# Kernel optimization log

Measured on AMD Instinct MI355X. Metric: run time of the kernel, lower is better.

The kernel has to match this reference:

```python
import jax, jax.numpy as jnp
import numpy as np

D_MODEL = 1024
N_LAYERS = 2
D_STATE = 64
D_CONV = 4
EXPAND = 2
D_INNER = EXPAND * D_MODEL            # 2048
HEADDIM = D_STATE                     # 64 (headdim=d_state per module code)
NHEADS = D_INNER // HEADDIM           # 32
CONV_DIM = D_INNER + 2 * D_STATE      # 2176 (ngroups=1)
D_IN_PROJ = 2 * D_INNER + 2 * D_STATE + NHEADS  # 4256
EPS = 1e-5


def setup_inputs() -> dict:
    key = jax.random.key(0)
    ks = jax.random.split(key, 8)
    B, L = 2, 4096
    return {
        "x": jax.random.normal(ks[0], (B, L, D_MODEL), jnp.float32),
        "ln_w": jnp.ones((N_LAYERS, D_MODEL), jnp.float32),
        "ln_b": jnp.zeros((N_LAYERS, D_MODEL), jnp.float32),
        "in_proj_w": jax.random.normal(ks[1], (N_LAYERS, D_IN_PROJ, D_MODEL), jnp.float32) * (D_MODEL ** -0.5),
        "conv_w": jax.random.normal(ks[2], (N_LAYERS, CONV_DIM, D_CONV), jnp.float32) * (D_CONV ** -0.5),
        "conv_b": jnp.zeros((N_LAYERS, CONV_DIM), jnp.float32),
        "dt_bias": jax.random.normal(ks[3], (N_LAYERS, NHEADS), jnp.float32) * 0.5,
        "A_log": jnp.log(jax.random.uniform(ks[4], (N_LAYERS, NHEADS), jnp.float32, 1.0, 16.0)),
        "D": jnp.ones((N_LAYERS, NHEADS), jnp.float32),
        "rms_w": jnp.ones((N_LAYERS, D_INNER), jnp.float32),
        "out_proj_w": jax.random.normal(ks[5], (N_LAYERS, D_MODEL, D_INNER), jnp.float32) * (D_INNER ** -0.5),
    }


def _layernorm(x, w, b):
    m = x.mean(-1, keepdims=True)
    v = ((x - m) ** 2).mean(-1, keepdims=True)
    return (x - m) * jax.lax.rsqrt(v + EPS) * w + b


def _mamba2(u, in_w, conv_w, conv_b, dt_bias, A_log, Dp, rms_w, out_w):
    b, l, _ = u.shape
    zxbcdt = u @ in_w.T                                   # (b,l,D_IN_PROJ)
    z, xBC, dt = jnp.split(zxbcdt, [D_INNER, D_INNER + CONV_DIM], axis=-1)
    dt = jax.nn.softplus(dt + dt_bias)                    # (b,l,H)
    # causal depthwise conv over sequence
    xBC = jnp.transpose(xBC, (0, 2, 1))                   # (b,C,l)
    xBC = jax.lax.conv_general_dilated(
        xBC, conv_w[:, None, :], (1,), [(D_CONV - 1, 0)],
        dimension_numbers=("NCH", "OIH", "NCH"), feature_group_count=CONV_DIM)
    xBC = jnp.transpose(xBC, (0, 2, 1)) + conv_b
    xBC = jax.nn.silu(xBC)
    xh, Bm, Cm = jnp.split(xBC, [D_INNER, D_INNER + D_STATE], axis=-1)
    xh = xh.reshape(b, l, NHEADS, HEADDIM)                # (b,l,H,P)
    A = -jnp.exp(A_log)                                   # (H,)
    dA = jnp.exp(dt * A)                                  # (b,l,H)

    def step(state, inputs):
        dA_t, dt_t, x_t, B_t, C_t = inputs                # (b,H),(b,H),(b,H,P),(b,N),(b,N)
        state = dA_t[:, :, None, None] * state + (dt_t[:, :, None] * x_t)[..., None] * B_t[:, None, None, :]
        y_t = jnp.einsum("bhpn,bn->bhp", state, C_t)
        return state, y_t

    xs = (jnp.moveaxis(dA, 1, 0), jnp.moveaxis(dt, 1, 0), jnp.moveaxis(xh, 1, 0),
          jnp.moveaxis(Bm, 1, 0), jnp.moveaxis(Cm, 1, 0))
    init = jnp.zeros((b, NHEADS, HEADDIM, D_STATE), u.dtype)
    _, ys = jax.lax.scan(step, init, xs)                  # ys: (l,b,H,P)
    y = jnp.moveaxis(ys, 0, 1) + Dp[None, None, :, None] * xh
    y = y.reshape(b, l, D_INNER)
    # gated RMSNorm (norm_before_gate=False): gate then rmsnorm
    y = y * jax.nn.silu(z)
    y = y * jax.lax.rsqrt(jnp.mean(y * y, -1, keepdims=True) + EPS) * rms_w
    return y @ out_w.T


def reference(x, ln_w, ln_b, in_proj_w, conv_w, conv_b, dt_bias, A_log, D, rms_w, out_proj_w):
    h = x
    for i in range(N_LAYERS):
        res = h
        h = _layernorm(h, ln_w[i], ln_b[i])
        h = _mamba2(h, in_proj_w[i], conv_w[i], conv_b[i], dt_bias[i], A_log[i], D[i], rms_w[i], out_proj_w[i])
        h = h + res
    return h
```

## Files before the change

kernel.cpp:

```cpp
#include <hip/hip_runtime.h>
#include <stdint.h>

#define D_MODEL   1024
#define D_STATE   64
#define D_INNER   2048
#define NHEADS    32
#define CONV_DIM  2176
#define D_IN_PROJ 4256
#define NPAD1     4352
#define LSEQ      4096
#define BL        8192
#define NCHUNK    32
#define TCH       128
#define EPS       1e-5f

typedef __attribute__((ext_vector_type(8))) _Float16 f16x8;
typedef __attribute__((ext_vector_type(4))) _Float16 f16x4;
typedef __attribute__((ext_vector_type(4))) float f32x4;

__device__ __forceinline__ void load_lds16(const void* g, void* l) {
  __builtin_amdgcn_global_load_lds((const __attribute__((address_space(1))) void*)g,
                                   (__attribute__((address_space(3))) void*)l, 16, 0, 0);
}

__global__ __launch_bounds__(256) void cvt_w1_kernel(const float* __restrict__ w,
                                                     _Float16* __restrict__ o) {
  size_t idx = (size_t)blockIdx.x * 256 + threadIdx.x;
  int k = idx & 1023;
  size_t nr = idx >> 10;
  int layer = (int)(nr / NPAD1);
  int n = (int)(nr % NPAD1);
  float v = (n < D_IN_PROJ) ? w[((size_t)layer * D_IN_PROJ + n) * 1024 + k] : 0.f;
  o[idx] = (_Float16)v;
}
__global__ __launch_bounds__(256) void cvt_w2_kernel(const float* __restrict__ w,
                                                     _Float16* __restrict__ o) {
  size_t idx = (size_t)blockIdx.x * 256 + threadIdx.x;
  o[idx] = (_Float16)w[idx];
}

__global__ __launch_bounds__(256) void ln_kernel(const float* __restrict__ x,
                                                 const float* __restrict__ w,
                                                 const float* __restrict__ b,
                                                 _Float16* __restrict__ o) {
  int row = blockIdx.x, tid = threadIdx.x;
  const float* xr = x + (size_t)row * D_MODEL;
  float4 v = *(const float4*)(xr + tid * 4);
  float s = v.x + v.y + v.z + v.w;
  float q = v.x * v.x + v.y * v.y + v.z * v.z + v.w * v.w;
  for (int off = 1; off < 64; off <<= 1) { s += __shfl_xor(s, off); q += __shfl_xor(q, off); }
  __shared__ float rs[4], rq[4];
  int wave = tid >> 6, lane = tid & 63;
  if (lane == 0) { rs[wave] = s; rq[wave] = q; }
  __syncthreads();
  s = rs[0] + rs[1] + rs[2] + rs[3];
  q = rq[0] + rq[1] + rq[2] + rq[3];
  float mean = s * (1.f / D_MODEL);
  float var = q * (1.f / D_MODEL) - mean * mean;
  float rstd = rsqrtf(var + EPS);
  int c = tid * 4;
  f16x4 ov;
  ov[0] = (_Float16)((v.x - mean) * rstd * w[c + 0] + b[c + 0]);
  ov[1] = (_Float16)((v.y - mean) * rstd * w[c + 1] + b[c + 1]);
  ov[2] = (_Float16)((v.z - mean) * rstd * w[c + 2] + b[c + 2]);
  ov[3] = (_Float16)((v.w - mean) * rstd * w[c + 3] + b[c + 3]);
  *(f16x4*)(o + (size_t)row * D_MODEL + c) = ov;
}

template <int MODE>
__global__ __launch_bounds__(512, 4) void gemm_f16_kernel(
    const _Float16* __restrict__ A, int lda,
    const _Float16* __restrict__ Bw, int K, int NBN,
    _Float16* __restrict__ Zb, _Float16* __restrict__ XPRE, float* __restrict__ AUX,
    float* __restrict__ Cf, const float* __restrict__ resid) {
  __shared__ _Float16 lA[2][256 * 32];
  __shared__ _Float16 lB[2][128 * 32];
  int tid = threadIdx.x;
  int wv = tid >> 6, lane = tid & 63;
  int nwg = gridDim.x;
  int cpx = nwg >> 3;
  int wg = ((int)blockIdx.x & 7) * cpx + ((int)blockIdx.x >> 3);
  int band = wg / (4 * NBN), rem = wg % (4 * NBN);
  int bm = band * 4 + (rem & 3);
  int bn = rem >> 2;

  const int wm = (wv >> 1) * 64, wn = (wv & 1) * 64;
  const int fr = lane & 15;
  const int s4 = lane >> 4;
  size_t aoff = (size_t)(bm * 256) * lda;
  size_t boff = (size_t)(bn * 128) * K;

  f32x4 acc[4][4];
  f32x4 zero = {0.f, 0.f, 0.f, 0.f};
#pragma unroll
  for (int i = 0; i < 4; ++i)
#pragma unroll
    for (int j = 0; j < 4; ++j) acc[i][j] = zero;

  auto stage = [&](int k0, int buf) {
#pragma unroll
    for (int c = 0; c < 2; ++c) {
      int row = (wv * 2 + c) * 16 + (lane >> 2);
      int col = k0 + (((lane & 3) ^ ((row >> 1) & 3)) << 3);
      load_lds16(A + aoff + (size_t)row * lda + col,
                 &lA[buf][(wv * 2 + c) * 512 + lane * 8]);
    }
    int rowb = wv * 16 + (lane >> 2);
    int colb = k0 + (((lane & 3) ^ ((rowb >> 1) & 3)) << 3);
    load_lds16(Bw + boff + (size_t)rowb * K + colb, &lB[buf][wv * 512 + lane * 8]);
  };

  int nk = K >> 5;
  stage(0, 0);
  for (int kk = 0; kk < nk; ++kk) {
    int cur = kk & 1;
    bool pf = (kk + 1 < nk);
    if (pf) {
      stage((kk + 1) << 5, cur ^ 1);
      asm volatile("s_waitcnt vmcnt(3)" ::: "memory");
    } else {
      asm volatile("s_waitcnt vmcnt(0)" ::: "memory");
    }
    __builtin_amdgcn_s_barrier();
    __builtin_amdgcn_sched_barrier(0);
    f16x8 af[4], bf[4];
#pragma unroll
    for (int i = 0; i < 4; ++i) {
      int R = wm + i * 16 + fr;
      af[i] = *(const f16x8*)&lA[cur][R * 32 + ((s4 ^ ((R >> 1) & 3)) << 3)];
    }
#pragma unroll
    for (int j = 0; j < 4; ++j) {
      int R = wn + j * 16 + fr;
      bf[j] = *(const f16x8*)&lB[cur][R * 32 + ((s4 ^ ((R >> 1) & 3)) << 3)];
    }
#pragma unroll
    for (int i = 0; i < 4; ++i)
#pragma unroll
      for (int j = 0; j < 4; ++j)
        acc[i][j] = __builtin_amdgcn_mfma_f32_16x16x32_f16(af[i], bf[j], acc[i][j], 0, 0, 0);
    __builtin_amdgcn_sched_barrier(0);
    __builtin_amdgcn_s_barrier();
  }

  int r0 = (lane >> 4) * 4;
  int cc = lane & 15;
#pragma unroll
  for (int i = 0; i < 4; ++i) {
#pragma unroll
    for (int j = 0; j < 4; ++j) {
      int col = bn * 128 + wn + j * 16 + cc;
#pragma unroll
      for (int r = 0; r < 4; ++r) {
        size_t row = (size_t)(bm * 256 + wm + i * 16 + r0 + r);
        float v = acc[i][j][r];
        if constexpr (MODE == 0) {
          if (col < 2048)       Zb[row * 2048 + col] = (_Float16)v;
          else if (col < 4096)  XPRE[row * 2048 + (col - 2048)] = (_Float16)v;
          else if (col < 4256)  AUX[row * 160 + (col - 4096)] = v;
        } else {
          size_t idx = row * 1024 + col;
          Cf[idx] = v + resid[idx];
        }
      }
    }
  }
}

__global__ __launch_bounds__(256) void dt_kernel(const float* __restrict__ aux,
                                                 const float* __restrict__ dtb,
                                                 const float* __restrict__ alog,
                                                 float* __restrict__ dtt,
                                                 float* __restrict__ dta) {
  int idx = blockIdx.x * 256 + threadIdx.x;
  int h = idx >> 13, l = idx & 8191;
  float A = -__expf(alog[h]);
  float v = aux[(size_t)l * 160 + 128 + h] + dtb[h];
  float sp = (v > 20.f) ? v : log1pf(expf(v));
  dtt[idx] = sp;
  dta[idx] = sp * A;
}

__global__ __launch_bounds__(128) void lc_kernel(const float* __restrict__ dta,
                                                 float* __restrict__ lco) {
  int bid = blockIdx.x;
  int h = bid >> 6, b = (bid >> 5) & 1, ct = bid & 31;
  size_t base = (size_t)h * BL + b * LSEQ + ct * TCH;
  int tid = threadIdx.x, lane = tid & 63;
  float v = dta[base + tid];
#pragma unroll
  for (int off = 1; off < 64; off <<= 1) {
    float o = __shfl_up(v, off);
    if (lane >= off) v += o;
  }
  __shared__ float tot;
  if (tid == 63) tot = v;
  __syncthreads();
  if (tid >= 64) v += tot;
  lco[base + tid] = v;
}

__global__ __launch_bounds__(256) void conv_kernel(const _Float16* __restrict__ xpre,
                                                   const float* __restrict__ aux,
                                                   const float* __restrict__ cw,
                                                   const float* __restrict__ cb,
                                                   _Float16* __restrict__ xh,
                                                   float* __restrict__ Bo,
                                                   float* __restrict__ Co) {
  int c = blockIdx.y * 256 + threadIdx.x;
  if (c >= CONV_DIM) return;
  int l0 = blockIdx.x * 16;
  float w0 = cw[c * 4 + 0], w1 = cw[c * 4 + 1], w2 = cw[c * 4 + 2], w3 = cw[c * 4 + 3];
  float bias = cb[c];
  bool isx = (c < 2048);
  auto ldx = [&](int l) -> float {
    return isx ? (float)xpre[(size_t)l * 2048 + c] : aux[(size_t)l * 160 + (c - 2048)];
  };
  float a0 = 0.f, a1 = 0.f, a2 = 0.f;
  if ((l0 & 4095) != 0) { a0 = ldx(l0 - 3); a1 = ldx(l0 - 2); a2 = ldx(l0 - 1); }
#pragma unroll
  for (int t = 0; t < 16; ++t) {
    int l = l0 + t;
    float a3 = ldx(l);
    float acc = bias + a0 * w0 + a1 * w1 + a2 * w2 + a3 * w3;
    acc = acc / (1.f + __expf(-acc));
    if (isx)
      xh[(size_t)l * 2048 + c] = (_Float16)acc;
    else if (c < 2112)
      Bo[(size_t)l * 64 + (c - 2048)] = acc;
    else
      Co[(size_t)l * 64 + (c - 2112)] = acc;
    a0 = a1; a1 = a2; a2 = a3;
  }
}

__global__ __launch_bounds__(256) void transpose_x_kernel(const _Float16* __restrict__ xh,
                                                          _Float16* __restrict__ xt) {
  __shared__ _Float16 T[64 * 65];
  int c0 = blockIdx.x * 64;
  int l0 = blockIdx.y * 64;
  int tid = threadIdx.x;
  int rr = tid >> 3, g8 = tid & 7;
#pragma unroll
  for (int p = 0; p < 2; ++p) {
    int l = p * 32 + rr;
    f16x8 v = *(const f16x8*)&xh[(size_t)(l0 + l) * 2048 + c0 + g8 * 8];
#pragma unroll
    for (int j = 0; j < 8; ++j) T[l * 65 + g8 * 8 + j] = v[j];
  }
  __syncthreads();
#pragma unroll
  for (int p = 0; p < 2; ++p) {
    int c = p * 32 + rr;
    f16x8 v;
#pragma unroll
    for (int j = 0; j < 8; ++j) v[j] = T[(g8 * 8 + j) * 65 + c];
    *(f16x8*)&xt[(size_t)(c0 + c) * 8192 + l0 + g8 * 8] = v;
  }
}

__global__ __launch_bounds__(256) void transpose_b_kernel(const float* __restrict__ bc,
                                                          _Float16* __restrict__ bt) {
  __shared__ _Float16 T[64 * 65];
  int l0 = blockIdx.x * 64;
  int tid = threadIdx.x;
  int rr4 = tid >> 4, cl = tid & 15;
#pragma unroll
  for (int p = 0; p < 4; ++p) {
    int l = p * 16 + rr4;
    float4 v = *(const float4*)&bc[(size_t)(l0 + l) * 64 + cl * 4];
    T[l * 65 + cl * 4 + 0] = (_Float16)v.x;
    T[l * 65 + cl * 4 + 1] = (_Float16)v.y;
    T[l * 65 + cl * 4 + 2] = (_Float16)v.z;
    T[l * 65 + cl * 4 + 3] = (_Float16)v.w;
  }
  __syncthreads();
  int rr = tid >> 3, g8 = tid & 7;
#pragma unroll
  for (int p = 0; p < 2; ++p) {
    int n = p * 32 + rr;
    f16x8 v;
#pragma unroll
    for (int j = 0; j < 8; ++j) v[j] = T[(g8 * 8 + j) * 65 + n];
    *(f16x8*)&bt[(size_t)n * 8192 + l0 + g8 * 8] = v;
  }
}

__global__ __launch_bounds__(256) void scan_state_kernel(
    const _Float16* __restrict__ xt, const _Float16* __restrict__ bt,
    const float* __restrict__ lc, const float* __restrict__ dtt,
    float* __restrict__ cs) {
  int bid = blockIdx.x;
  int chunk = bid & 31, h = (bid >> 5) & 31, b = bid >> 10;
  int tid = threadIdx.x;
  size_t gb = (size_t)b * LSEQ + chunk * TCH;
  size_t cdb = (size_t)h * BL + gb;
  __shared__ _Float16 xtl[64 * 128];
  __shared__ _Float16 btl[64 * 128];
  __shared__ float ldsW[128];
  if (tid < 128) ldsW[tid] = dtt[cdb + tid] * __expf(lc[cdb + 127] - lc[cdb + tid]);
  __syncthreads();
  int rr = tid >> 4, cl = tid & 15;
#pragma unroll
  for (int p = 0; p < 4; ++p) {
    int row = p * 16 + rr;
    f16x8 v = *(const f16x8*)&xt[(size_t)(h * 64 + row) * BL + gb + cl * 8];
    f16x8 bv = *(const f16x8*)&bt[(size_t)row * BL + gb + cl * 8];
    f16x8 sv;
#pragma unroll
    for (int j = 0; j < 8; ++j) sv[j] = (_Float16)((float)v[j] * ldsW[cl * 8 + j]);
    int byo = (row * 256 + cl * 16) ^ ((row & 7) << 4);
    *(f16x8*)((char*)xtl + byo) = sv;
    *(f16x8*)((char*)btl + byo) = bv;
  }
  __syncthreads();
  int wv = tid >> 6, lane = tid & 63;
  int fr = lane & 15, fk = (lane >> 4) * 8, r0 = (lane >> 4) * 4, cc = lane & 15;
  int swz = (fr & 7) << 4;
  f32x4 acc[4];
  f32x4 zero = {0.f, 0.f, 0.f, 0.f};
#pragma unroll
  for (int j = 0; j < 4; ++j) acc[j] = zero;
#pragma unroll
  for (int k0 = 0; k0 < 128; k0 += 32) {
    f16x8 af = *(const f16x8*)((char*)xtl + (((wv * 16 + fr) * 256 + (k0 + fk) * 2) ^ swz));
#pragma unroll
    for (int j = 0; j < 4; ++j) {
      f16x8 bf = *(const f16x8*)((char*)btl + (((j * 16 + fr) * 256 + (k0 + fk) * 2) ^ swz));
      acc[j] = __builtin_amdgcn_mfma_f32_16x16x32_f16(af, bf, acc[j], 0, 0, 0);
    }
  }
  size_t cbase = (((size_t)(b * 32 + h) * 32) + chunk) * 4096;
#pragma unroll
  for (int j = 0; j < 4; ++j)
#pragma unroll
    for (int r = 0; r < 4; ++r)
      cs[cbase + (wv * 16 + r0 + r) * 64 + j * 16 + cc] = acc[j][r];
}

__global__ __launch_bounds__(256) void scan_p2_kernel(float* __restrict__ cs,
                                                      const float* __restrict__ lc) {
  int bid = blockIdx.x;
  int b = bid >> 7, h = (bid >> 2) & 31, pq = bid & 3;
  int tid = threadIdx.x;
  size_t base = ((size_t)(b * 32 + h) * 32) * 4096 + (size_t)(pq * 256 + tid) * 4;
  const float* lcd = lc + (size_t)h * BL + b * LSEQ;
  float4 s = {0.f, 0.f, 0.f, 0.f};
  for (int c = 0; c < NCHUNK; ++c) {
    size_t idx = base + (size_t)c * 4096;
    float4 e = *(const float4*)&cs[idx];
    float P = __expf(lcd[c * TCH + TCH - 1]);
    *(float4*)&cs[idx] = s;
    s.x = e.x + P * s.x;
    s.y = e.y + P * s.y;
    s.z = e.z + P * s.z;
    s.w = e.w + P * s.w;
  }
}

__global__ __launch_bounds__(256) void scan_y_kernel(
    const _Float16* __restrict__ xt, const float* __restrict__ Cc,
    const float* __restrict__ Bc, const float* __restrict__ cs,
    const float* __restrict__ lc, const float* __restrict__ dtt,
    const float* __restrict__ Dv, float* __restrict__ y) {
  int bid = blockIdx.x;
  int chunk = bid & 31, h = (bid >> 5) & 31, b = bid >> 10;
  int tid = threadIdx.x;
  size_t gb = (size_t)b * LSEQ + chunk * TCH;
  size_t cdb = (size_t)h * BL + gb;

  __shared__ _Float16 uCB[2 * 128 * 64];
  __shared__ _Float16 xtl[64 * 128];
  __shared__ _Float16 spl[64 * 64];
  __shared__ float ldsLc[128];
  __shared__ float ldsDt[128];
  _Float16* Cl = uCB;
  _Float16* Bl = uCB + 128 * 64;
  _Float16* Pl = uCB;

  int rr = tid >> 4, cl = tid & 15;
#pragma unroll
  for (int p = 0; p < 8; ++p) {
    int row = p * 16 + rr;
    float4 cv = *(const float4*)&Cc[(gb + row) * 64 + cl * 4];
    float4 bv = *(const float4*)&Bc[(gb + row) * 64 + cl * 4];
    f16x4 ch = {(_Float16)cv.x, (_Float16)cv.y, (_Float16)cv.z, (_Float16)cv.w};
    f16x4 bh = {(_Float16)bv.x, (_Float16)bv.y, (_Float16)bv.z, (_Float16)bv.w};
    int byo = (row * 128 + cl * 8) ^ ((row & 7) << 4);
    *(f16x4*)((char*)Cl + byo) = ch;
    *(f16x4*)((char*)Bl + byo) = bh;
  }
  size_t cbase = (((size_t)(b * 32 + h) * 32) + chunk) * 4096;
#pragma unroll
  for (int p = 0; p < 4; ++p) {
    int row = p * 16 + rr;
    f16x8 v = *(const f16x8*)&xt[(size_t)(h * 64 + row) * BL + gb + cl * 8];
    int byo = (row * 256 + cl * 16) ^ ((row & 7) << 4);
    *(f16x8*)((char*)xtl + byo) = v;
    float4 sv = *(const float4*)&cs[cbase + row * 64 + cl * 4];
    f16x4 sh = {(_Float16)sv.x, (_Float16)sv.y, (_Float16)sv.z, (_Float16)sv.w};
    int byo2 = (row * 128 + cl * 8) ^ ((row & 7) << 4);
    *(f16x4*)((char*)spl + byo2) = sh;
  }
  if (tid < 128) { ldsLc[tid] = lc[cdb + tid]; ldsDt[tid] = dtt[cdb + tid]; }
  __syncthreads();

  int wv = tid >> 6, lane = tid & 63;
  int fr = lane & 15, fk = (lane >> 4) * 8, r0 = (lane >> 4) * 4, cc = lane & 15;
  int tb = wv * 32;
  int swz = (fr & 7) << 4;

  f32x4 accY[2][4];
  f32x4 accS[2][8];
  f32x4 zero = {0.f, 0.f, 0.f, 0.f};
#pragma unroll
  for (int i = 0; i < 2; ++i) {
#pragma unroll
    for (int j = 0; j < 4; ++j) accY[i][j] = zero;
#pragma unroll
    for (int j = 0; j < 8; ++j) accS[i][j] = zero;
  }

#pragma unroll
  for (int k0 = 0; k0 < 64; k0 += 32) {
    f16x8 ac[2];
#pragma unroll
    for (int i = 0; i < 2; ++i)
      ac[i] = *(const f16x8*)((char*)Cl + (((tb + i * 16 + fr) * 128 + (k0 + fk) * 2) ^ swz));
#pragma unroll
    for (int j = 0; j < 4; ++j) {
      f16x8 bs = *(const f16x8*)((char*)spl + (((j * 16 + fr) * 128 + (k0 + fk) * 2) ^ swz));
#pragma unroll
      for (int i = 0; i < 2; ++i)
        accY[i][j] = __builtin_amdgcn_mfma_f32_16x16x32_f16(ac[i], bs, accY[i][j], 0, 0, 0);
    }
#pragma unroll
    for (int j = 0; j < 8; ++j) {
      f16x8 bb = *(const f16x8*)((char*)Bl + (((j * 16 + fr) * 128 + (k0 + fk) * 2) ^ swz));
#pragma unroll
      for (int i = 0; i < 2; ++i)
        accS[i][j] = __builtin_amdgcn_mfma_f32_16x16x32_f16(ac[i], bb, accS[i][j], 0, 0, 0);
    }
  }

  float lct[2][4];
#pragma unroll
  for (int i = 0; i < 2; ++i)
#pragma unroll
    for (int r = 0; r < 4; ++r) lct[i][r] = ldsLc[tb + i * 16 + r0 + r];
#pragma unroll
  for (int i = 0; i < 2; ++i)
#pragma unroll
    for (int r = 0; r < 4; ++r) {
      float sc = __expf(lct[i][r]);
#pragma unroll
      for (int j = 0; j < 4; ++j) accY[i][j][r] *= sc;
    }

  __syncthreads();
  float Dh = Dv[h];
#pragma unroll
  for (int i = 0; i < 2; ++i)
#pragma unroll
    for (int jj = 0; jj < 8; ++jj) {
      int s = jj * 16 + cc;
      float lcs = ldsLc[s];
      float dts = ldsDt[s];
#pragma unroll
      for (int r = 0; r < 4; ++r) {
        int t = tb + i * 16 + r0 + r;
        float v = 0.f;
        if (s <= t) v = accS[i][jj][r] * __expf(lct[i][r] - lcs) * dts;
        if (s == t) v += Dh;
        int byo = (t * 256 + s * 2) ^ ((t & 7) << 4);
        *(_Float16*)((char*)Pl + byo) = (_Float16)v;
      }
    }
  __syncthreads();

#pragma unroll
  for (int k0 = 0; k0 < 128; k0 += 32) {
    f16x8 ap[2];
#pragma unroll
    for (int i = 0; i < 2; ++i)
      ap[i] = *(const f16x8*)((char*)Pl + (((tb + i * 16 + fr) * 256 + (k0 + fk) * 2) ^ swz));
#pragma unroll
    for (int j = 0; j < 4; ++j) {
      f16x8 bx = *(const f16x8*)((char*)xtl + (((j * 16 + fr) * 256 + (k0 + fk) * 2) ^ swz));
#pragma unroll
      for (int i = 0; i < 2; ++i)
        accY[i][j] = __builtin_amdgcn_mfma_f32_16x16x32_f16(ap[i], bx, accY[i][j], 0, 0, 0);
    }
  }

#pragma unroll
  for (int i = 0; i < 2; ++i)
#pragma unroll
    for (int j = 0; j < 4; ++j)
#pragma unroll
      for (int r = 0; r < 4; ++r) {
        int t = tb + i * 16 + r0 + r;
        y[(gb + t) * 2048 + h * 64 + j * 16 + cc] = accY[i][j][r];
      }
}

__global__ __launch_bounds__(256) void gate_rms_kernel(const float* __restrict__ yf,
                                                       const _Float16* __restrict__ zb,
                                                       const float* __restrict__ rw,
                                                       _Float16* __restrict__ g) {
  int row = blockIdx.x, tid = threadIdx.x;
  const float* yr = yf + (size_t)row * D_INNER;
  const _Float16* zr = zb + (size_t)row * D_INNER;
  float gv[8];
  float q = 0.f;
#pragma unroll
  for (int u = 0; u < 8; ++u) {
    int c = u * 256 + tid;
    float yv = yr[c];
    float zv = (float)zr[c];
    float t = yv * (zv / (1.f + __expf(-zv)));
    gv[u] = t;
    q += t * t;
  }
  for (int off = 1; off < 64; off <<= 1) q += __shfl_xor(q, off);
  __shared__ float rq[4];
  if ((tid & 63) == 0) rq[tid >> 6] = q;
  __syncthreads();
  q = rq[0] + rq[1] + rq[2] + rq[3];
  float scale = rsqrtf(q * (1.f / D_INNER) + EPS);
  _Float16* gr = g + (size_t)row * D_INNER;
#pragma unroll
  for (int u = 0; u < 8; ++u) {
    int c = u * 256 + tid;
    gr[c] = (_Float16)(gv[u] * scale * rw[c]);
  }
}

extern "C" void kernel_launch(void* const* d_in, const int* in_sizes, int n_in,
                              void* d_out, int out_size, void* d_ws, size_t ws_size,
                              hipStream_t stream) {
  (void)in_sizes; (void)n_in; (void)out_size; (void)ws_size;
  const float* x     = (const float*)d_in[0];
  const float* ln_w  = (const float*)d_in[1];
  const float* ln_b  = (const float*)d_in[2];
  const float* w_in  = (const float*)d_in[3];
  const float* cw    = (const float*)d_in[4];
  const float* cb    = (const float*)d_in[5];
  const float* dtb   = (const float*)d_in[6];
  const float* alog  = (const float*)d_in[7];
  const float* dvec  = (const float*)d_in[8];
  const float* rmsw  = (const float*)d_in[9];
  const float* w_out = (const float*)d_in[10];
  float* out = (float*)d_out;

  char* ws = (char*)d_ws;
  size_t off = 0;
  auto alloc = [&](size_t bytes) -> char* {
    char* p = ws + off;
    off += (bytes + 255) & ~(size_t)255;
    return p;
  };
  _Float16* W1 = (_Float16*)alloc(2ull * 2 * NPAD1 * 1024);
  _Float16* W2 = (_Float16*)alloc(2ull * 2 * 1024 * 2048);
  char* REGION = alloc(4ull * BL * D_INNER);
  _Float16* LNf = (_Float16*)REGION;
  float* Yf = (float*)REGION;
  _Float16* Zb = (_Float16*)alloc(2ull * BL * D_INNER);
  _Float16* XPRE = (_Float16*)alloc(2ull * BL * D_INNER);
  _Float16* XT = XPRE;
  _Float16* XH = (_Float16*)alloc(2ull * BL * D_INNER);
  float* AUX  = (float*)alloc(4ull * BL * 160);
  float* BC = (float*)alloc(4ull * BL * D_STATE);
  float* CC = (float*)alloc(4ull * BL * D_STATE);
  float* DTt = (float*)alloc(4ull * NHEADS * BL);
  float* DTA = (float*)alloc(4ull * NHEADS * BL);
  float* LC  = (float*)alloc(4ull * NHEADS * BL);
  _Float16* BT = (_Float16*)alloc(2ull * D_STATE * BL);
  float* CS = (float*)alloc(4ull * 2 * NHEADS * NCHUNK * 4096);

  cvt_w1_kernel<<<(2 * NPAD1 * 1024) / 256, 256, 0, stream>>>(w_in, W1);
  cvt_w2_kernel<<<(2 * 1024 * 2048) / 256, 256, 0, stream>>>(w_out, W2);

  for (int layer = 0; layer < 2; ++layer) {
    const float* hin = layer ? (const float*)out : x;
    size_t o1 = (size_t)layer * NPAD1 * 1024;
    size_t o2 = (size_t)layer * 1024 * 2048;
    ln_kernel<<<BL, 256, 0, stream>>>(hin, ln_w + layer * D_MODEL, ln_b + layer * D_MODEL, LNf);
    gemm_f16_kernel<0><<<dim3((8192 / 256) * (NPAD1 / 128)), 512, 0, stream>>>(
        LNf, 1024, W1 + o1, 1024, NPAD1 / 128, Zb, XPRE, AUX, nullptr, nullptr);
    dt_kernel<<<(NHEADS * BL) / 256, 256, 0, stream>>>(AUX, dtb + layer * NHEADS,
                                                       alog + layer * NHEADS, DTt, DTA);
    lc_kernel<<<2048, 128, 0, stream>>>(DTA, LC);
    conv_kernel<<<dim3(BL / 16, 9), 256, 0, stream>>>(XPRE, AUX, cw + layer * CONV_DIM * 4,
                                                      cb + layer * CONV_DIM, XH, BC, CC);
    transpose_x_kernel<<<dim3(32, 128), 256, 0, stream>>>(XH, XT);
    transpose_b_kernel<<<128, 256, 0, stream>>>(BC, BT);
    scan_state_kernel<<<2048, 256, 0, stream>>>(XT, BT, LC, DTt, CS);
    scan_p2_kernel<<<256, 256, 0, stream>>>(CS, LC);
    scan_y_kernel<<<2048, 256, 0, stream>>>(XT, CC, BC, CS, LC, DTt,
                                            dvec + layer * NHEADS, Yf);
    gate_rms_kernel<<<BL, 256, 0, stream>>>(Yf, Zb, rmsw + layer * D_INNER, Zb);
    gemm_f16_kernel<1><<<dim3((8192 / 256) * (1024 / 128)), 512, 0, stream>>>(
        Zb, 2048, W2 + o2, 2048, 1024 / 128, nullptr, nullptr, nullptr, out, hin);
  }
}
```

Baseline: 782.2 us.

## Triple-buffer GEMM LDS staging and fuse dt softplus with chunk cumsum

The GEMM main loop goes from double to triple buffering in LDS. It prefetches two K-steps ahead and waits with vmcnt(6) so global loads have more time to land before each tile is consumed. Separately, the dt softplus kernel and the per-chunk cumulative-sum kernel are merged into one, which removes the DTA intermediate buffer and one launch. The deeper buffering raises LDS per block from 48KB to 72KB, which may lower occupancy below the requested 4 blocks per CU.

```diff
diff --git a/kernel.cpp b/kernel.cpp
--- a/kernel.cpp
+++ b/kernel.cpp
@@ -73,8 +73,8 @@
     const _Float16* __restrict__ Bw, int K, int NBN,
     _Float16* __restrict__ Zb, _Float16* __restrict__ XPRE, float* __restrict__ AUX,
     float* __restrict__ Cf, const float* __restrict__ resid) {
-  __shared__ _Float16 lA[2][256 * 32];
-  __shared__ _Float16 lB[2][128 * 32];
+  __shared__ _Float16 lA[3][256 * 32];
+  __shared__ _Float16 lB[3][128 * 32];
   int tid = threadIdx.x;
   int wv = tid >> 6, lane = tid & 63;
   int nwg = gridDim.x;
@@ -112,11 +112,14 @@
 
   int nk = K >> 5;
   stage(0, 0);
+  stage(32, 1);
+  int cur = 0;
   for (int kk = 0; kk < nk; ++kk) {
-    int cur = kk & 1;
-    bool pf = (kk + 1 < nk);
-    if (pf) {
-      stage((kk + 1) << 5, cur ^ 1);
+    if (kk + 2 < nk) {
+      int sb = cur + 2; if (sb >= 3) sb -= 3;
+      stage((kk + 2) << 5, sb);
+      asm volatile("s_waitcnt vmcnt(6)" ::: "memory");
+    } else if (kk + 1 < nk) {
       asm volatile("s_waitcnt vmcnt(3)" ::: "memory");
     } else {
       asm volatile("s_waitcnt vmcnt(0)" ::: "memory");
@@ -141,6 +144,7 @@
         acc[i][j] = __builtin_amdgcn_mfma_f32_16x16x32_f16(af[i], bf[j], acc[i][j], 0, 0, 0);
     __builtin_amdgcn_sched_barrier(0);
     __builtin_amdgcn_s_barrier();
+    cur = cur + 1; if (cur >= 3) cur = 0;
   }
 
   int r0 = (lane >> 4) * 4;
@@ -167,37 +171,31 @@
   }
 }
 
-__global__ __launch_bounds__(256) void dt_kernel(const float* __restrict__ aux,
-                                                 const float* __restrict__ dtb,
-                                                 const float* __restrict__ alog,
-                                                 float* __restrict__ dtt,
-                                                 float* __restrict__ dta) {
-  int idx = blockIdx.x * 256 + threadIdx.x;
-  int h = idx >> 13, l = idx & 8191;
+__global__ __launch_bounds__(128) void dtlc_kernel(const float* __restrict__ aux,
+                                                   const float* __restrict__ dtb,
+                                                   const float* __restrict__ alog,
+                                                   float* __restrict__ dtt,
+                                                   float* __restrict__ lco) {
+  int bid = blockIdx.x;
+  int h = bid >> 6, b = (bid >> 5) & 1, ct = bid & 31;
+  int tid = threadIdx.x, lane = tid & 63;
+  int l = b * LSEQ + ct * TCH + tid;
   float A = -__expf(alog[h]);
   float v = aux[(size_t)l * 160 + 128 + h] + dtb[h];
   float sp = (v > 20.f) ? v : log1pf(expf(v));
-  dtt[idx] = sp;
-  dta[idx] = sp * A;
-}
-
-__global__ __launch_bounds__(128) void lc_kernel(const float* __restrict__ dta,
-                                                 float* __restrict__ lco) {
-  int bid = blockIdx.x;
-  int h = bid >> 6, b = (bid >> 5) & 1, ct = bid & 31;
   size_t base = (size_t)h * BL + b * LSEQ + ct * TCH;
-  int tid = threadIdx.x, lane = tid & 63;
-  float v = dta[base + tid];
+  dtt[base + tid] = sp;
+  float d = sp * A;
 #pragma unroll
   for (int off = 1; off < 64; off <<= 1) {
-    float o = __shfl_up(v, off);
-    if (lane >= off) v += o;
+    float o = __shfl_up(d, off);
+    if (lane >= off) d += o;
   }
   __shared__ float tot;
-  if (tid == 63) tot = v;
-  __syncthreads();
-  if (tid >= 64) v += tot;
-  lco[base + tid] = v;
+  if (tid == 63) tot = d;
+  __syncthreads();
+  if (tid >= 64) d += tot;
+  lco[base + tid] = d;
 }
 
 __global__ __launch_bounds__(256) void conv_kernel(const _Float16* __restrict__ xpre,
@@ -573,7 +571,6 @@
   float* BC = (float*)alloc(4ull * BL * D_STATE);
   float* CC = (float*)alloc(4ull * BL * D_STATE);
   float* DTt = (float*)alloc(4ull * NHEADS * BL);
-  float* DTA = (float*)alloc(4ull * NHEADS * BL);
   float* LC  = (float*)alloc(4ull * NHEADS * BL);
   _Float16* BT = (_Float16*)alloc(2ull * D_STATE * BL);
   float* CS = (float*)alloc(4ull * 2 * NHEADS * NCHUNK * 4096);
@@ -588,9 +585,8 @@
     ln_kernel<<<BL, 256, 0, stream>>>(hin, ln_w + layer * D_MODEL, ln_b + layer * D_MODEL, LNf);
     gemm_f16_kernel<0><<<dim3((8192 / 256) * (NPAD1 / 128)), 512, 0, stream>>>(
         LNf, 1024, W1 + o1, 1024, NPAD1 / 128, Zb, XPRE, AUX, nullptr, nullptr);
-    dt_kernel<<<(NHEADS * BL) / 256, 256, 0, stream>>>(AUX, dtb + layer * NHEADS,
-                                                       alog + layer * NHEADS, DTt, DTA);
-    lc_kernel<<<2048, 128, 0, stream>>>(DTA, LC);
+    dtlc_kernel<<<2048, 128, 0, stream>>>(AUX, dtb + layer * NHEADS,
+                                          alog + layer * NHEADS, DTt, LC);
     conv_kernel<<<dim3(BL / 16, 9), 256, 0, stream>>>(XPRE, AUX, cw + layer * CONV_DIM * 4,
                                                       cb + layer * CONV_DIM, XH, BC, CC);
     transpose_x_kernel<<<dim3(32, 128), 256, 0, stream>>>(XH, XT);
```

Result: no change. 783.3 us (+0.1%).
